# Performance work log

Measured on AMD Instinct MI355X. Metric: run time of the kernel, lower is better.

The kernel has to match this reference:

```python
import jax, jax.numpy as jnp
import numpy as np
from jax import lax

# LiteMSA config: in_ch=256, out_ch=256, dim=8, heads=32, total_dim=256, scales=(3,)
DIM = 8
QKV_CH = 768          # 3 * total_dim
PW_GROUPS = 96        # 3 * heads


def setup_inputs() -> dict:
    key = jax.random.key(0)
    ks = jax.random.split(key, 5)
    x = jax.random.normal(ks[0], (16, 256, 64, 64), jnp.float32)
    w_qkv = jax.random.normal(ks[1], (768, 256), jnp.float32) * 0.02      # 1x1 conv
    w_dw = jax.random.normal(ks[2], (768, 1, 3, 3), jnp.float32) * 0.02   # depthwise 3x3
    w_pw = jax.random.normal(ks[3], (768, 8, 1, 1), jnp.float32) * 0.02   # grouped 1x1, 96 groups
    w_proj = jax.random.normal(ks[4], (256, 512), jnp.float32) * 0.02     # 1x1 conv
    bn_gamma = jnp.ones((256,), jnp.float32)
    bn_beta = jnp.zeros((256,), jnp.float32)
    bn_mean = jnp.zeros((256,), jnp.float32)
    bn_var = jnp.ones((256,), jnp.float32)
    return {"x": x, "w_qkv": w_qkv, "w_dw": w_dw, "w_pw": w_pw, "w_proj": w_proj,
            "bn_gamma": bn_gamma, "bn_beta": bn_beta, "bn_mean": bn_mean, "bn_var": bn_var}


def reference(x, w_qkv, w_dw, w_pw, w_proj, bn_gamma, bn_beta, bn_mean, bn_var):
    B, _, H, W = x.shape
    dn = ("NCHW", "OIHW", "NCHW")
    # qkv 1x1 conv
    qkv = jnp.einsum("bchw,oc->bohw", x, w_qkv)  # [B,768,H,W]
    # multi-scale aggregation: depthwise 3x3 -> grouped 1x1
    agg = lax.conv_general_dilated(qkv, w_dw, (1, 1), "SAME",
                                   dimension_numbers=dn, feature_group_count=QKV_CH)
    agg = lax.conv_general_dilated(agg, w_pw, (1, 1), "SAME",
                                   dimension_numbers=dn, feature_group_count=PW_GROUPS)
    ms = jnp.concatenate([qkv, agg], axis=1)  # [B,1536,H,W]
    # [B, heads_total=64, N=H*W, 3*dim]
    ms = ms.reshape(B, -1, 3 * DIM, H * W).transpose(0, 1, 3, 2)
    q = jax.nn.relu(ms[..., :DIM])
    k = jax.nn.relu(ms[..., DIM:2 * DIM])
    v = ms[..., 2 * DIM:]
    # pad v with ones for normalizer channel
    v = jnp.concatenate([v, jnp.ones(v.shape[:-1] + (1,), v.dtype)], axis=-1)  # [B,h,N,dim+1]
    kv = jnp.einsum("bhnd,bhne->bhde", k, v)   # [B,h,dim,dim+1]
    out = jnp.einsum("bhnd,bhde->bhne", q, kv)  # [B,h,N,dim+1]
    out = out[..., :DIM] / (out[..., DIM:] + 1e-15)
    out = out.transpose(0, 1, 3, 2).reshape(B, -1, H, W)  # [B,512,H,W]
    # proj 1x1 conv + BatchNorm (inference, running stats)
    y = jnp.einsum("bchw,oc->bohw", out, w_proj)
    inv = bn_gamma / jnp.sqrt(bn_var + 1e-5)
    y = y * inv[None, :, None, None] + (bn_beta - bn_mean * inv)[None, :, None, None]
    return y
```

## Files before the change

### kernel.cpp

```cpp
#include <hip/hip_runtime.h>
#include <hip/hip_bf16.h>


#define NB 16
#define CQKV 768
#define P4096 4096

typedef __bf16 bf16x8 __attribute__((ext_vector_type(8)));
typedef float f32x4 __attribute__((ext_vector_type(4)));

#define MFMA_BF16 __builtin_amdgcn_mfma_f32_16x16x32_bf16

__device__ __forceinline__ ushort f2bf(float f) {
    union { float f; unsigned int u; } x; x.f = f;
    unsigned int u = x.u;
    unsigned int r = (u + 0x7FFFu + ((u >> 16) & 1u)) >> 16;
    return (ushort)r;
}
__device__ __forceinline__ float bf2f(ushort u) {
    union { unsigned int u; float f; } x; x.u = ((unsigned int)u) << 16;
    return x.f;
}
__device__ __forceinline__ unsigned int pk2bf(float x, float y) {
    __hip_bfloat162 h = __float22bfloat162_rn(make_float2(x, y));
    union { __hip_bfloat162 b; unsigned int u; } c; c.b = h; return c.u;
}
__device__ __forceinline__ void stage_hi8(const float* v, ushort* dh) {
    union { unsigned int u[4]; uint4 q; } H;
    #pragma unroll
    for (int i = 0; i < 4; i++) H.u[i] = pk2bf(v[2 * i], v[2 * i + 1]);
    *(uint4*)dh = H.q;
}

__device__ __forceinline__ void gload16(void* lds, const void* g) {
    __builtin_amdgcn_global_load_lds(
        (const __attribute__((address_space(1))) void*)g,
        (__attribute__((address_space(3))) void*)lds, 16, 0, 0);
}

__global__ __launch_bounds__(128) void conv_w(
    const float* __restrict__ W, ushort* __restrict__ Ah, ushort* __restrict__ Al)
{
    const int rv = blockIdx.x;
    const int t  = threadIdx.x;
    int phys;
    if (rv < 256) phys = (rv >> 3) * 24 + (rv & 7);
    else { int r2 = rv - 256; phys = (r2 >> 4) * 24 + 8 + (r2 & 15); }
    int c = t * 2;
    float w0 = W[(size_t)phys * 256 + c];
    float w1 = W[(size_t)phys * 256 + c + 1];
    unsigned int h = pk2bf(w0, w1);
    float f0 = __uint_as_float(h << 16);
    float f1 = __uint_as_float(h & 0xffff0000u);
    unsigned int l = pk2bf(w0 - f0, w1 - f1);
    int sl = ((c >> 3) & 3) ^ ((rv >> 1) & 3);
    int idx = (c & ~31) + sl * 8 + (c & 7);
    *(unsigned int*)&Ah[(size_t)rv * 256 + idx] = h;
    *(unsigned int*)&Al[(size_t)rv * 256 + idx] = l;
}

__global__ __launch_bounds__(256) void conv_x(
    const float* __restrict__ X, ushort* __restrict__ XTh, ushort* __restrict__ XTl)
{
    const int pt = blockIdx.x;
    const int ct = blockIdx.y;
    const int b  = blockIdx.z;
    const int t  = threadIdx.x;
    const int p0 = pt * 64, c0 = ct * 64;

    __shared__ float tile[64][65];

    {
        int cr = t >> 2, pc = (t & 3) * 16;
        const float* xr = X + ((size_t)b * 256 + c0 + cr) * P4096 + p0 + pc;
        float4 v0 = *(const float4*)xr;
        float4 v1 = *(const float4*)(xr + 4);
        float4 v2 = *(const float4*)(xr + 8);
        float4 v3 = *(const float4*)(xr + 12);
        float* d = &tile[cr][pc];
        d[0]=v0.x; d[1]=v0.y; d[2]=v0.z; d[3]=v0.w;
        d[4]=v1.x; d[5]=v1.y; d[6]=v1.z; d[7]=v1.w;
        d[8]=v2.x; d[9]=v2.y; d[10]=v2.z; d[11]=v2.w;
        d[12]=v3.x; d[13]=v3.y; d[14]=v3.z; d[15]=v3.w;
    }
    __syncthreads();

    #pragma unroll
    for (int pass = 0; pass < 2; pass++) {
        int tp = t >> 2;
        int cc = (t & 3) + pass * 4;
        int p  = p0 + tp;
        float v[8];
        #pragma unroll
        for (int j = 0; j < 8; j++) v[j] = tile[cc * 8 + j][tp];
        union { unsigned int u[4]; uint4 q; } H, L;
        #pragma unroll
        for (int i = 0; i < 4; i++) {
            unsigned int h = pk2bf(v[2 * i], v[2 * i + 1]);
            H.u[i] = h;
            float f0 = __uint_as_float(h << 16);
            float f1 = __uint_as_float(h & 0xffff0000u);
            L.u[i] = pk2bf(v[2 * i] - f0, v[2 * i + 1] - f1);
        }
        int c = c0 + cc * 8;
        int sl = ((c >> 3) & 3) ^ ((p >> 1) & 3);
        size_t idx = ((size_t)b * P4096 + p) * 256 + (c & ~31) + sl * 8;
        *(uint4*)&XTh[idx] = H.q;
        *(uint4*)&XTl[idx] = L.q;
    }
}

__global__ __launch_bounds__(256, 3) void gemm_fused(
    const ushort* __restrict__ Ah, const ushort* __restrict__ Al,
    const ushort* __restrict__ Bh, const ushort* __restrict__ Bl,
    ushort* __restrict__ Cbf, float* __restrict__ qplane)
{
    const int mt = blockIdx.x;
    const int n0 = blockIdx.y * 128;
    const int b  = blockIdx.z;
    const int t  = threadIdx.x;
    const int wave = t >> 6, lane = t & 63, quad = lane >> 4, l15 = lane & 15;
    const int wr = wave >> 1, wc = wave & 1;
    const int M0 = mt * 128;

    __shared__ __align__(16) ushort AsH[128 * 32];
    __shared__ __align__(16) ushort AsL[128 * 32];
    __shared__ __align__(16) ushort BsH[128 * 32];
    __shared__ __align__(16) ushort BsL[128 * 32];

    int aoff[4], boff[4];
    #pragma unroll
    for (int i = 0; i < 4; i++) {
        int ra = wr * 64 + i * 16 + l15;
        aoff[i] = ra * 64 + ((quad ^ ((ra >> 1) & 3)) << 4);
        int rb = wc * 64 + i * 16 + l15;
        boff[i] = rb * 64 + ((quad ^ ((rb >> 1) & 3)) << 4);
    }

    const int srow = t >> 2;
    const int schunk = (t & 3) * 8;
    const size_t abase = (size_t)(M0 + srow) * 256 + schunk;
    const size_t bbase = ((size_t)b * P4096 + n0 + srow) * 256 + schunk;
    const int ldsoff = wave * 1024;

    f32x4 acc[4][4];
    #pragma unroll
    for (int mi = 0; mi < 4; mi++)
        #pragma unroll
        for (int nj = 0; nj < 4; nj++)
            #pragma unroll
            for (int r = 0; r < 4; r++) acc[mi][nj][r] = 0.0f;

    if (mt < 2) {
        for (int kw = 0; kw < 8; kw++) {
            __syncthreads();
            #pragma unroll
            for (int i = 0; i < 2; i++) {
                int lo = ldsoff + i * 4096;
                size_t so = (size_t)(i * 64) * 256 + kw * 32;
                gload16((char*)AsH + lo, Ah + abase + so);
                gload16((char*)AsL + lo, Al + abase + so);
                gload16((char*)BsH + lo, Bh + bbase + so);
                gload16((char*)BsL + lo, Bl + bbase + so);
            }
            __syncthreads();
            bf16x8 ah[4], al[4];
            #pragma unroll
            for (int mi = 0; mi < 4; mi++) {
                ah[mi] = *(const bf16x8*)((const char*)AsH + aoff[mi]);
                al[mi] = *(const bf16x8*)((const char*)AsL + aoff[mi]);
            }
            #pragma unroll
            for (int nj = 0; nj < 4; nj++) {
                bf16x8 bh = *(const bf16x8*)((const char*)BsH + boff[nj]);
                bf16x8 bl = *(const bf16x8*)((const char*)BsL + boff[nj]);
                #pragma unroll
                for (int mi = 0; mi < 4; mi++) {
                    acc[mi][nj] = MFMA_BF16(ah[mi], bh, acc[mi][nj], 0, 0, 0);
                    acc[mi][nj] = MFMA_BF16(al[mi], bh, acc[mi][nj], 0, 0, 0);
                    acc[mi][nj] = MFMA_BF16(ah[mi], bl, acc[mi][nj], 0, 0, 0);
                }
            }
        }
        #pragma unroll
        for (int mi = 0; mi < 4; mi++)
            #pragma unroll
            for (int nj = 0; nj < 4; nj++)
                #pragma unroll
                for (int r = 0; r < 4; r++) {
                    int rv = M0 + wr * 64 + mi * 16 + quad * 4 + r;
                    int rp = (rv >> 3) * 24 + (rv & 7);
                    int col = n0 + wc * 64 + nj * 16 + l15;
                    float v = acc[mi][nj][r];
                    Cbf[((size_t)b * CQKV + rp) * P4096 + col] = f2bf(v);
                    qplane[((size_t)b * 256 + rv) * P4096 + col] = v;
                }
    } else {
        for (int kw = 0; kw < 8; kw++) {
            __syncthreads();
            #pragma unroll
            for (int i = 0; i < 2; i++) {
                int lo = ldsoff + i * 4096;
                size_t so = (size_t)(i * 64) * 256 + kw * 32;
                gload16((char*)AsH + lo, Ah + abase + so);
                gload16((char*)BsH + lo, Bh + bbase + so);
            }
            __syncthreads();
            bf16x8 ah[4];
            #pragma unroll
            for (int mi = 0; mi < 4; mi++)
                ah[mi] = *(const bf16x8*)((const char*)AsH + aoff[mi]);
            #pragma unroll
            for (int nj = 0; nj < 4; nj++) {
                bf16x8 bh = *(const bf16x8*)((const char*)BsH + boff[nj]);
                #pragma unroll
                for (int mi = 0; mi < 4; mi++)
                    acc[mi][nj] = MFMA_BF16(ah[mi], bh, acc[mi][nj], 0, 0, 0);
            }
        }
        #pragma unroll
        for (int mi = 0; mi < 4; mi++)
            #pragma unroll
            for (int nj = 0; nj < 4; nj++)
                #pragma unroll
                for (int r = 0; r < 4; r++) {
                    int rv2 = (M0 - 256) + wr * 64 + mi * 16 + quad * 4 + r;
                    int rp = (rv2 >> 4) * 24 + 8 + (rv2 & 15);
                    int col = n0 + wc * 64 + nj * 16 + l15;
                    Cbf[((size_t)b * CQKV + rp) * P4096 + col] = f2bf(acc[mi][nj][r]);
                }
    }
}

__global__ __launch_bounds__(256) void qfix_kernel(
    float* __restrict__ qplane, const float* __restrict__ w_qkv,
    const float* __restrict__ x)
{
    size_t i = (size_t)blockIdx.x * 256 + threadIdx.x;
    float q = qplane[i];
    if (fabsf(q) >= 1e-4f) return;
    int p   = (int)(i & 4095);
    int qch = (int)((i >> 12) & 255);
    int b   = (int)(i >> 20);
    int row = (qch >> 3) * 24 + (qch & 7);
    const float* wr = w_qkv + (size_t)row * 256;
    const float* xr = x + (size_t)b * 256 * P4096 + p;
    double s = 0.0;
    for (int c = 0; c < 256; c++)
        s += (double)wr[c] * (double)xr[(size_t)c * P4096];
    qplane[i] = (float)s;
}

__global__ __launch_bounds__(512, 8) void dwpw_kernel(
    const ushort* __restrict__ qkv, const float* __restrict__ wdw,
    const float* __restrict__ wpw, ushort* __restrict__ agg)
{
    const int rt = blockIdx.x;
    const int g  = blockIdx.y;
    const int b  = blockIdx.z;
    const int t  = threadIdx.x;
    const int r0 = rt * 16;
    const int cg = g * 8;

    __shared__ __align__(16) ushort tile[8][18][80];

    const ushort* src = qkv + ((size_t)(b * CQKV + cg)) * P4096;

    if (t < 288) {
        int ch = t / 36;
        int rr = (t % 36) >> 1;
        int side = t & 1;
        *(uint4*)&tile[ch][rr][side * 72] = make_uint4(0, 0, 0, 0);
    }
    #pragma unroll
    for (int i = 0; i < 3; i++) {
        int id = t + i * 512;
        if (id < 1152) {
            int ch  = id / 144;
            int rem = id - ch * 144;
            int rr  = rem >> 3;
            int oct = (rem & 7) * 8;
            int grow = r0 - 1 + rr;
            uint4 v = make_uint4(0, 0, 0, 0);
            if (grow >= 0 && grow < 64)
                v = *(const uint4*)(src + (size_t)ch * P4096 + (size_t)grow * 64 + oct);
            *(uint4*)&tile[ch][rr][8 + oct] = v;
        }
    }
    __syncthreads();

    const int kc  = t & 31;
    const int row = t >> 5;
    const float* wdwg = wdw + (size_t)cg * 9;
    const float* wpwg = wpw + (size_t)cg * 8;

    float acc0[8], acc1[8];
    #pragma unroll
    for (int oi = 0; oi < 8; oi++) { acc0[oi] = 0.0f; acc1[oi] = 0.0f; }

    #pragma unroll
    for (int c = 0; c < 8; c++) {
        float dv0 = 0.0f, dv1 = 0.0f;
        #pragma unroll
        for (int dy = 0; dy < 3; dy++) {
            const ushort* rp = &tile[c][row + dy][2 * kc + 4];
            unsigned int u1 = *(const unsigned int*)(rp + 2);
            unsigned int u2 = *(const unsigned int*)(rp + 4);
            unsigned int u3 = *(const unsigned int*)(rp + 6);
            float xm1 = __uint_as_float(u1 & 0xffff0000u);
            float x0  = __uint_as_float(u2 << 16);
            float x1  = __uint_as_float(u2 & 0xffff0000u);
            float x2  = __uint_as_float(u3 << 16);
            float w0 = wdwg[c * 9 + dy * 3 + 0];
            float w1 = wdwg[c * 9 + dy * 3 + 1];
            float w2 = wdwg[c * 9 + dy * 3 + 2];
            dv0 = fmaf(w0, xm1, dv0); dv0 = fmaf(w1, x0, dv0); dv0 = fmaf(w2, x1, dv0);
            dv1 = fmaf(w0, x0,  dv1); dv1 = fmaf(w1, x1, dv1); dv1 = fmaf(w2, x2, dv1);
        }
        #pragma unroll
        for (int oi = 0; oi < 8; oi++) {
            float w = wpwg[oi * 8 + c];
            acc0[oi] = fmaf(w, dv0, acc0[oi]);
            acc1[oi] = fmaf(w, dv1, acc1[oi]);
        }
    }

    size_t obase = ((size_t)(b * CQKV + cg)) * P4096 + (size_t)(r0 + row) * 64 + 2 * kc;
    #pragma unroll
    for (int oi = 0; oi < 8; oi++) {
        unsigned int u = (unsigned int)f2bf(acc0[oi]) |
                         ((unsigned int)f2bf(acc1[oi]) << 16);
        *(unsigned int*)&agg[obase + (size_t)oi * P4096] = u;
    }
}

__global__ __launch_bounds__(256) void kv_kernel(
    const ushort* __restrict__ qkv, const ushort* __restrict__ agg,
    float* __restrict__ kv)
{
    const int h = blockIdx.x, b = blockIdx.y, t = threadIdx.x;
    const ushort* src = (h < 32)
        ? qkv + ((size_t)(b * CQKV + h * 24)) * P4096
        : agg + ((size_t)(b * CQKV + (h - 32) * 24)) * P4096;

    float acc[72];
    #pragma unroll
    for (int i = 0; i < 72; i++) acc[i] = 0.0f;

    for (int pi = 0; pi < 16; pi++) {
        int p = t + pi * 256;
        float kvv[8], vv[8];
        #pragma unroll
        for (int d = 0; d < 8; d++) {
            float xk = bf2f(src[(size_t)(8 + d) * P4096 + p]);
            kvv[d] = xk > 0.0f ? xk : 0.0f;
        }
        #pragma unroll
        for (int e = 0; e < 8; e++) vv[e] = bf2f(src[(size_t)(16 + e) * P4096 + p]);
        #pragma unroll
        for (int d = 0; d < 8; d++) {
            #pragma unroll
            for (int e = 0; e < 8; e++) acc[d * 9 + e] += kvv[d] * vv[e];
            acc[d * 9 + 8] += kvv[d];
        }
    }

    #pragma unroll
    for (int i = 0; i < 72; i++) {
        float v = acc[i];
        #pragma unroll
        for (int off = 32; off > 0; off >>= 1) v += __shfl_xor(v, off, 64);
        acc[i] = v;
    }
    __shared__ float part[4][72];
    int wave = t >> 6, lane = t & 63;
    if (lane == 0) {
        #pragma unroll
        for (int i = 0; i < 72; i++) part[wave][i] = acc[i];
    }
    __syncthreads();
    if (t < 72)
        kv[((size_t)b * 64 + h) * 72 + t] = part[0][t] + part[1][t] + part[2][t] + part[3][t];
}

__global__ __launch_bounds__(256) void attn_out_kernel(
    const float* __restrict__ qplane, ushort* __restrict__ agg,
    const float* __restrict__ kv)
{
    const int pt = blockIdx.x, h = blockIdx.y, b = blockIdx.z, t = threadIdx.x;
    __shared__ float kvs[72];
    if (t < 72) kvs[t] = kv[((size_t)b * 64 + h) * 72 + t];
    __syncthreads();

    const bool lohead = (h < 32);
    const float* srcf = lohead
        ? qplane + ((size_t)(b * 256 + h * 8)) * P4096 : nullptr;
    const ushort* srcb = lohead ? nullptr
        : agg + ((size_t)(b * CQKV + (h - 32) * 24)) * P4096;

    int p = pt * 256 + t;
    float num[8]; float den = 0.0f;
    #pragma unroll
    for (int e = 0; e < 8; e++) num[e] = 0.0f;
    #pragma unroll
    for (int d = 0; d < 8; d++) {
        float q = lohead ? srcf[(size_t)d * P4096 + p]
                         : bf2f(srcb[(size_t)d * P4096 + p]);
        q = q > 0.0f ? q : 0.0f;
        #pragma unroll
        for (int e = 0; e < 8; e++) num[e] += q * kvs[d * 9 + e];
        den += q * kvs[d * 9 + 8];
    }
    float rd = 1.0f / (den + 1e-15f);
    ushort* dst = agg + ((size_t)(b * CQKV + (h / 2) * 24 + 8 + (h % 2) * 8)) * P4096 + p;
    #pragma unroll
    for (int e = 0; e < 8; e++)
        dst[(size_t)e * P4096] = f2bf(num[e] * rd);
}

__global__ __launch_bounds__(256) void gemm_proj(
    const float* __restrict__ A,
    const ushort* __restrict__ Bagg,
    float* __restrict__ Y,
    const float* __restrict__ bn_g, const float* __restrict__ bn_b,
    const float* __restrict__ bn_m, const float* __restrict__ bn_v)
{
    const int n0 = blockIdx.x * 64;
    const int m0 = blockIdx.y * 64;
    const int b  = blockIdx.z;
    const int t  = threadIdx.x;
    const int wave = t >> 6, lane = t & 63, quad = lane >> 4, l15 = lane & 15;

    __shared__ __align__(16) ushort As[64][40];
    __shared__ __align__(16) ushort Bs[64][40];

    f32x4 acc[4];
    #pragma unroll
    for (int nt = 0; nt < 4; nt++)
        #pragma unroll
        for (int r = 0; r < 4; r++) acc[nt][r] = 0.0f;

    const int am = t >> 2, ak = (t & 3) * 8;
    const int bn = t & 63, kg = (t >> 6) * 8;

    for (int k0 = 0; k0 < 512; k0 += 32) {
        float av[8];
        *(float4*)&av[0] = *(const float4*)(A + (size_t)(m0 + am) * 512 + k0 + ak);
        *(float4*)&av[4] = *(const float4*)(A + (size_t)(m0 + am) * 512 + k0 + ak + 4);
        ushort bu[8];
        #pragma unroll
        for (int i = 0; i < 8; i++) {
            int kk = k0 + kg + i;
            int amch = (kk >> 4) * 24 + 8 + (kk & 15);
            bu[i] = Bagg[((size_t)b * CQKV + amch) * P4096 + n0 + bn];
        }

        __syncthreads();
        stage_hi8(av, &As[am][ak]);
        {
            union { ushort us[8]; uint4 q; } Bp;
            #pragma unroll
            for (int i = 0; i < 8; i++) Bp.us[i] = bu[i];
            *(uint4*)&Bs[bn][kg] = Bp.q;
        }
        __syncthreads();

        bf16x8 af = *(const bf16x8*)&As[wave * 16 + l15][quad * 8];
        #pragma unroll
        for (int nt = 0; nt < 4; nt++) {
            bf16x8 bf = *(const bf16x8*)&Bs[nt * 16 + l15][quad * 8];
            acc[nt] = MFMA_BF16(af, bf, acc[nt], 0, 0, 0);
        }
    }

    #pragma unroll
    for (int nt = 0; nt < 4; nt++) {
        #pragma unroll
        for (int r = 0; r < 4; r++) {
            int row = m0 + wave * 16 + quad * 4 + r;
            int col = n0 + nt * 16 + l15;
            float inv = bn_g[row] / sqrtf(bn_v[row] + 1e-5f);
            float v = acc[nt][r] * inv + (bn_b[row] - bn_m[row] * inv);
            Y[((size_t)b * 256 + row) * P4096 + col] = v;
        }
    }
}

extern "C" void kernel_launch(void* const* d_in, const int* in_sizes, int n_in,
                              void* d_out, int out_size, void* d_ws, size_t ws_size,
                              hipStream_t stream) {
    const float* x      = (const float*)d_in[0];
    const float* w_qkv  = (const float*)d_in[1];
    const float* w_dw   = (const float*)d_in[2];
    const float* w_pw   = (const float*)d_in[3];
    const float* w_proj = (const float*)d_in[4];
    const float* bn_g   = (const float*)d_in[5];
    const float* bn_b   = (const float*)d_in[6];
    const float* bn_m   = (const float*)d_in[7];
    const float* bn_v   = (const float*)d_in[8];
    float* y = (float*)d_out;

    char* ws = (char*)d_ws;
    ushort* qkv_bf = (ushort*)(ws);
    float*  qplane = (float*) (ws + 100663296);
    ushort* agg_bf = (ushort*)(ws + 167772160);
    ushort* XTh = (ushort*)(ws + 167772160);
    ushort* XTl = (ushort*)(ws + 167772160 + 33554432);
    ushort* Awh = (ushort*)(ws + 167772160 + 67108864);
    ushort* Awl = (ushort*)(ws + 167772160 + 67108864 + 393216);
    float*  kvbuf  = (float*)d_out;

    conv_w<<<dim3(768), 128, 0, stream>>>(w_qkv, Awh, Awl);
    conv_x<<<dim3(64, 4, NB), 256, 0, stream>>>(x, XTh, XTl);

    gemm_fused<<<dim3(6, 32, NB), 256, 0, stream>>>(
        Awh, Awl, XTh, XTl, qkv_bf, qplane);

    qfix_kernel<<<65536, 256, 0, stream>>>(qplane, w_qkv, x);

    dwpw_kernel<<<dim3(4, 96, NB), 512, 0, stream>>>(qkv_bf, w_dw, w_pw, agg_bf);

    kv_kernel<<<dim3(64, NB), 256, 0, stream>>>(qkv_bf, agg_bf, kvbuf);

    attn_out_kernel<<<dim3(16, 64, NB), 256, 0, stream>>>(qplane, agg_bf, kvbuf);

    gemm_proj<<<dim3(64, 4, NB), 256, 0, stream>>>(
        w_proj, agg_bf, y, bn_g, bn_b, bn_m, bn_v);
}
```

Baseline: 451.3 us.

## Double-buffer LDS tiles in QKV GEMM and remap block index for XCD locality

The QKV GEMM now keeps two LDS buffers per operand and prefetches the next K slice while the current one feeds the MFMAs, leaving one barrier per iteration instead of two. The 3D grid becomes a flat 3072-block grid whose index is remapped so that consecutive logical tiles fall on the same XCD, aiming for better L2 reuse of the shared X and W tiles. Doubling LDS to 64KB forces launch bounds down to 2 blocks per CU, so occupancy drops.

Result: no change. 445.8 us (-1.2%).

```diff
diff --git a/kernel.cpp b/kernel.cpp
--- a/kernel.cpp
+++ b/kernel.cpp
@@ -110,23 +110,26 @@
     }
 }
 
-__global__ __launch_bounds__(256, 3) void gemm_fused(
+__global__ __launch_bounds__(256, 2) void gemm_fused(
     const ushort* __restrict__ Ah, const ushort* __restrict__ Al,
     const ushort* __restrict__ Bh, const ushort* __restrict__ Bl,
     ushort* __restrict__ Cbf, float* __restrict__ qplane)
 {
-    const int mt = blockIdx.x;
-    const int n0 = blockIdx.y * 128;
-    const int b  = blockIdx.z;
+    const int hw = blockIdx.x;
+    const int lg = (hw & 7) * 384 + (hw >> 3);
+    const int mt = lg % 6;
+    const int rem = lg / 6;
+    const int n0 = (rem & 31) * 128;
+    const int b  = rem >> 5;
     const int t  = threadIdx.x;
     const int wave = t >> 6, lane = t & 63, quad = lane >> 4, l15 = lane & 15;
     const int wr = wave >> 1, wc = wave & 1;
     const int M0 = mt * 128;
 
-    __shared__ __align__(16) ushort AsH[128 * 32];
-    __shared__ __align__(16) ushort AsL[128 * 32];
-    __shared__ __align__(16) ushort BsH[128 * 32];
-    __shared__ __align__(16) ushort BsL[128 * 32];
+    __shared__ __align__(16) ushort AsH[2][4096];
+    __shared__ __align__(16) ushort AsL[2][4096];
+    __shared__ __align__(16) ushort BsH[2][4096];
+    __shared__ __align__(16) ushort BsL[2][4096];
 
     int aoff[4], boff[4];
     #pragma unroll
@@ -152,28 +155,32 @@
             for (int r = 0; r < 4; r++) acc[mi][nj][r] = 0.0f;
 
     if (mt < 2) {
-        for (int kw = 0; kw < 8; kw++) {
-            __syncthreads();
+        auto stageQ = [&](int d, int kw) {
             #pragma unroll
             for (int i = 0; i < 2; i++) {
                 int lo = ldsoff + i * 4096;
-                size_t so = (size_t)(i * 64) * 256 + kw * 32;
-                gload16((char*)AsH + lo, Ah + abase + so);
-                gload16((char*)AsL + lo, Al + abase + so);
-                gload16((char*)BsH + lo, Bh + bbase + so);
-                gload16((char*)BsL + lo, Bl + bbase + so);
+                size_t so = (size_t)(i * 64) * 256 + (size_t)kw * 32;
+                gload16((char*)AsH[d] + lo, Ah + abase + so);
+                gload16((char*)AsL[d] + lo, Al + abase + so);
+                gload16((char*)BsH[d] + lo, Bh + bbase + so);
+                gload16((char*)BsL[d] + lo, Bl + bbase + so);
             }
-            __syncthreads();
+        };
+        stageQ(0, 0);
+        __syncthreads();
+        for (int kw = 0; kw < 8; kw++) {
+            int cur = kw & 1;
+            if (kw < 7) stageQ(cur ^ 1, kw + 1);
             bf16x8 ah[4], al[4];
             #pragma unroll
             for (int mi = 0; mi < 4; mi++) {
-                ah[mi] = *(const bf16x8*)((const char*)AsH + aoff[mi]);
-                al[mi] = *(const bf16x8*)((const char*)AsL + aoff[mi]);
+                ah[mi] = *(const bf16x8*)((const char*)AsH[cur] + aoff[mi]);
+                al[mi] = *(const bf16x8*)((const char*)AsL[cur] + aoff[mi]);
             }
             #pragma unroll
             for (int nj = 0; nj < 4; nj++) {
-                bf16x8 bh = *(const bf16x8*)((const char*)BsH + boff[nj]);
-                bf16x8 bl = *(const bf16x8*)((const char*)BsL + boff[nj]);
+                bf16x8 bh = *(const bf16x8*)((const char*)BsH[cur] + boff[nj]);
+                bf16x8 bl = *(const bf16x8*)((const char*)BsL[cur] + boff[nj]);
                 #pragma unroll
                 for (int mi = 0; mi < 4; mi++) {
                     acc[mi][nj] = MFMA_BF16(ah[mi], bh, acc[mi][nj], 0, 0, 0);
@@ -181,6 +188,7 @@
                     acc[mi][nj] = MFMA_BF16(ah[mi], bl, acc[mi][nj], 0, 0, 0);
                 }
             }
+            __syncthreads();
         }
         #pragma unroll
         for (int mi = 0; mi < 4; mi++)
@@ -196,27 +204,32 @@
                     qplane[((size_t)b * 256 + rv) * P4096 + col] = v;
                 }
     } else {
-        for (int kw = 0; kw < 8; kw++) {
-            __syncthreads();
+        auto stageKV = [&](int d, int kw) {
             #pragma unroll
             for (int i = 0; i < 2; i++) {
                 int lo = ldsoff + i * 4096;
-                size_t so = (size_t)(i * 64) * 256 + kw * 32;
-                gload16((char*)AsH + lo, Ah + abase + so);
-                gload16((char*)BsH + lo, Bh + bbase + so);
+                size_t so = (size_t)(i * 64) * 256 + (size_t)kw * 32;
+                gload16((char*)AsH[d] + lo, Ah + abase + so);
+                gload16((char*)BsH[d] + lo, Bh + bbase + so);
             }
-            __syncthreads();
+        };
+        stageKV(0, 0);
+        __syncthreads();
+        for (int kw = 0; kw < 8; kw++) {
+            int cur = kw & 1;
+            if (kw < 7) stageKV(cur ^ 1, kw + 1);
             bf16x8 ah[4];
             #pragma unroll
             for (int mi = 0; mi < 4; mi++)
-                ah[mi] = *(const bf16x8*)((const char*)AsH + aoff[mi]);
+                ah[mi] = *(const bf16x8*)((const char*)AsH[cur] + aoff[mi]);
             #pragma unroll
             for (int nj = 0; nj < 4; nj++) {
-                bf16x8 bh = *(const bf16x8*)((const char*)BsH + boff[nj]);
+                bf16x8 bh = *(const bf16x8*)((const char*)BsH[cur] + boff[nj]);
                 #pragma unroll
                 for (int mi = 0; mi < 4; mi++)
                     acc[mi][nj] = MFMA_BF16(ah[mi], bh, acc[mi][nj], 0, 0, 0);
             }
+            __syncthreads();
         }
         #pragma unroll
         for (int mi = 0; mi < 4; mi++)
@@ -513,7 +526,7 @@
     conv_w<<<dim3(768), 128, 0, stream>>>(w_qkv, Awh, Awl);
     conv_x<<<dim3(64, 4, NB), 256, 0, stream>>>(x, XTh, XTl);
 
-    gemm_fused<<<dim3(6, 32, NB), 256, 0, stream>>>(
+    gemm_fused<<<dim3(3072), 256, 0, stream>>>(
         Awh, Awl, XTh, XTl, qkv_bf, qplane);
 
     qfix_kernel<<<65536, 256, 0, stream>>>(qplane, w_qkv, x);
```
